# Performance work log

Measured on AMD Instinct MI355X. Metric: run time of the kernel, lower is better.

Reference implementation:

```python
import jax, jax.numpy as jnp
import numpy as np

N_CLASS = 100
HIDDEN = 768
BATCH = 512


def setup_inputs() -> dict:
    key = jax.random.key(0)
    kx, ky, km = jax.random.split(key, 3)
    x = jax.random.normal(kx, (BATCH, HIDDEN), dtype=jnp.float32)
    y = jax.random.randint(ky, (BATCH,), 0, N_CLASS, dtype=jnp.int64 if jax.config.jax_enable_x64 else jnp.int32)
    M = jax.random.normal(km, (N_CLASS, HIDDEN, HIDDEN), dtype=jnp.float32) * 0.1
    return {"x": x, "y": y, "M": M}


def _get_sym_M(M):
    # M: [n_class, H, H]
    h = M.shape[-1]
    Mt = jnp.triu(M)
    diag = Mt * jnp.eye(h, dtype=M.dtype)  # keeps only diagonal entries
    # detached ReLU correction: pushes near-zero/negative diagonal up by ~0.001
    Mt = Mt + jax.lax.stop_gradient(jax.nn.relu(-(diag - 0.001)))
    return jnp.einsum('chk,cjk->chj', Mt, Mt)  # Mt @ Mt^T, symmetric PSD


def reference(x, y, M):
    # Faithful to: one_hot(y) broadcast-select of sym_M then batched matvec.
    # Equivalent efficient form: gather selected class matrix, per-sample matvec.
    sym = _get_sym_M(M)            # [n_class, H, H]
    My = sym[y]                    # [B, H, H] gather (irregular access)
    return jnp.einsum('bh,bhk->bk', x, My)  # [B, H]
```

## Files before the change

### kernel.cpp

```cpp
#include <hip/hip_runtime.h>

#define NCLASS 100
#define HID    768
#define BATCH  512
#define SG     8
#define NPAN   12

__device__ __forceinline__ void build_list(const int* __restrict__ y, int c,
                                           int* slist, int* scnt, int t) {
    if (t < 64) {
        int n = 0;
        for (int r = 0; r < BATCH / 64; ++r) {
            const int b = r * 64 + t;
            const bool hit = (y[b] == c);
            const unsigned long long mask = __ballot(hit);
            if (hit) slist[n + __popcll(mask & ((1ull << t) - 1ull))] = b;
            n += __popcll(mask);
        }
        if (t == 0) *scnt = n;
    }
}

__global__ __launch_bounds__(256, 4) void kA(
    const float* __restrict__ x, const int* __restrict__ y,
    const float* __restrict__ M, float* __restrict__ T)
{
    const int c    = blockIdx.x;
    const int g    = (NPAN - 1) - blockIdx.y;
    const int t    = threadIdx.x;
    const int col0 = g * 64;

    __shared__ int   slist[BATCH];
    __shared__ int   scnt;
    __shared__ float xs[SG][HID];
    __shared__ float Xs[SG];
    __shared__ float red[4][16][4][SG];
    __shared__ float dj_lds[64];

    build_list(y, c, slist, &scnt, t);
    __syncthreads();
    const int cnt = scnt;
    if (cnt == 0) return;

    const float* __restrict__ Mc = M + (size_t)c * HID * HID;
    const int wv = t >> 6, ln = t & 63;
    const int hg = t >> 4, jq = t & 15;

    if (t < 64) {
        const int jg = col0 + t;
        dj_lds[t] = fmaxf(Mc[(size_t)jg * HID + jg], 1e-3f);
    }

    for (int g0 = 0; g0 < cnt; g0 += SG) {
        const int gs = min(SG, cnt - g0);
        __syncthreads();
        #pragma unroll
        for (int ss = 0; ss < 2; ++ss) {
            const int s = 2 * wv + ss;
            const int b = slist[g0 + (s < gs ? s : 0)];
            const float4* xr = (const float4*)(x + (size_t)b * HID);
            const float4 v0 = xr[ln], v1 = xr[ln + 64], v2 = xr[ln + 128];
            *(float4*)&xs[s][ln * 4]       = v0;
            *(float4*)&xs[s][ln * 4 + 256] = v1;
            *(float4*)&xs[s][ln * 4 + 512] = v2;
            float pX = ((v0.x + v0.y) + (v0.z + v0.w))
                     + ((v1.x + v1.y) + (v1.z + v1.w))
                     + ((v2.x + v2.y) + (v2.z + v2.w));
            #pragma unroll
            for (int off = 32; off; off >>= 1) pX += __shfl_xor(pX, off);
            if (ln == 0) Xs[s] = pX;
        }
        __syncthreads();

        float tp[4][SG];
        #pragma unroll
        for (int jj = 0; jj < 4; ++jj)
            #pragma unroll
            for (int s = 0; s < SG; ++s) tp[jj][s] = 0.f;

        for (int h = hg; h < col0 + 64; h += 16) {
            float4 mq = *(const float4*)(Mc + (size_t)h * HID + col0 + jq * 4);
            if (h >= col0) {
                const int hrel = h - col0;
                if (4 * jq + 0 <= hrel) mq.x = 0.f;
                if (4 * jq + 1 <= hrel) mq.y = 0.f;
                if (4 * jq + 2 <= hrel) mq.z = 0.f;
                if (4 * jq + 3 <= hrel) mq.w = 0.f;
            }
            #pragma unroll
            for (int s = 0; s < SG; ++s) {
                const float xv = xs[s][h];
                tp[0][s] = fmaf(xv, mq.x, tp[0][s]);
                tp[1][s] = fmaf(xv, mq.y, tp[1][s]);
                tp[2][s] = fmaf(xv, mq.z, tp[2][s]);
                tp[3][s] = fmaf(xv, mq.w, tp[3][s]);
            }
        }
        #pragma unroll
        for (int m = 16; m <= 32; m <<= 1)
            #pragma unroll
            for (int jj = 0; jj < 4; ++jj)
                #pragma unroll
                for (int s = 0; s < SG; ++s)
                    tp[jj][s] += __shfl_xor(tp[jj][s], m);
        if (ln < 16) {
            #pragma unroll
            for (int jj = 0; jj < 4; ++jj)
                #pragma unroll
                for (int s = 0; s < SG; ++s)
                    red[wv][ln][jj][s] = tp[jj][s];
        }
        __syncthreads();
        {
            const int j = t & 63, jq2 = j >> 2, jj2 = j & 3;
            const int jg = col0 + j;
            #pragma unroll
            for (int ss = 0; ss < 2; ++ss) {
                const int s = (t >> 6) * 2 + ss;
                if (s < gs) {
                    const float u = (red[0][jq2][jj2][s] + red[1][jq2][jj2][s])
                                  + (red[2][jq2][jj2][s] + red[3][jq2][jj2][s]);
                    const float xj = xs[s][jg];
                    T[(size_t)slist[g0 + s] * HID + jg] =
                        u + dj_lds[j] * xj + 1e-3f * (Xs[s] - xj);
                }
            }
        }
    }
}

__global__ __launch_bounds__(256, 4) void kB(
    const int* __restrict__ y, const float* __restrict__ M,
    const float* __restrict__ T, float* __restrict__ out)
{
    const int c  = blockIdx.x;
    const int q  = blockIdx.y;
    const int t  = threadIdx.x;
    const int k0 = q * 64;

    __shared__ int   slist[BATCH];
    __shared__ int   scnt;
    __shared__ float ts[SG][HID];
    __shared__ float Tt[SG];
    __shared__ float ob[SG][64];
    __shared__ float dk_lds[64];

    build_list(y, c, slist, &scnt, t);
    __syncthreads();
    const int cnt = scnt;
    if (cnt == 0) return;

    const float* __restrict__ Mc = M + (size_t)c * HID * HID;
    const int wv = t >> 6, ln = t & 63;
    const int kr = t >> 4, cg = t & 15;

    if (t < 64) {
        const int kg = k0 + t;
        dk_lds[t] = fmaxf(Mc[(size_t)kg * HID + kg], 1e-3f);
    }

    for (int g0 = 0; g0 < cnt; g0 += SG) {
        const int gs = min(SG, cnt - g0);
        __syncthreads();
        #pragma unroll
        for (int ss = 0; ss < 2; ++ss) {
            const int s = 2 * wv + ss;
            const int b = slist[g0 + (s < gs ? s : 0)];
            const float4* tr = (const float4*)(T + (size_t)b * HID);
            const float4 v0 = tr[ln], v1 = tr[ln + 64], v2 = tr[ln + 128];
            *(float4*)&ts[s][ln * 4]       = v0;
            *(float4*)&ts[s][ln * 4 + 256] = v1;
            *(float4*)&ts[s][ln * 4 + 512] = v2;
            float pT = ((v0.x + v0.y) + (v0.z + v0.w))
                     + ((v1.x + v1.y) + (v1.z + v1.w))
                     + ((v2.x + v2.y) + (v2.z + v2.w));
            #pragma unroll
            for (int off = 32; off; off >>= 1) pT += __shfl_xor(pT, off);
            if (ln == 0) Tt[s] = pT;
        }
        __syncthreads();

        float acc[4][SG];
        #pragma unroll
        for (int m = 0; m < 4; ++m)
            #pragma unroll
            for (int s = 0; s < SG; ++s) acc[m][s] = 0.f;

        for (int jb = k0; jb < HID; jb += 64) {
            const int j0 = jb + cg * 4;
            float4 mq[4];
            #pragma unroll
            for (int m = 0; m < 4; ++m) {
                const int k = k0 + 16 * m + kr;
                mq[m] = *(const float4*)(Mc + (size_t)k * HID + j0);
                if (jb == k0) {
                    if (j0 + 0 <= k) mq[m].x = 0.f;
                    if (j0 + 1 <= k) mq[m].y = 0.f;
                    if (j0 + 2 <= k) mq[m].z = 0.f;
                    if (j0 + 3 <= k) mq[m].w = 0.f;
                }
            }
            #pragma unroll
            for (int s = 0; s < SG; ++s) {
                const float4 tv = *(const float4*)&ts[s][j0];
                #pragma unroll
                for (int m = 0; m < 4; ++m) {
                    acc[m][s] = fmaf(mq[m].x, tv.x, acc[m][s]);
                    acc[m][s] = fmaf(mq[m].y, tv.y, acc[m][s]);
                    acc[m][s] = fmaf(mq[m].z, tv.z, acc[m][s]);
                    acc[m][s] = fmaf(mq[m].w, tv.w, acc[m][s]);
                }
            }
        }
        #pragma unroll
        for (int m2 = 1; m2 <= 8; m2 <<= 1)
            #pragma unroll
            for (int m = 0; m < 4; ++m)
                #pragma unroll
                for (int s = 0; s < SG; ++s)
                    acc[m][s] += __shfl_xor(acc[m][s], m2);
        if (cg == 0) {
            #pragma unroll
            for (int m = 0; m < 4; ++m)
                #pragma unroll
                for (int s = 0; s < SG; ++s)
                    ob[s][16 * m + kr] = acc[m][s];
        }
        __syncthreads();
        {
            const int j = t & 63;
            const int k = k0 + j;
            #pragma unroll
            for (int ss = 0; ss < 2; ++ss) {
                const int s = (t >> 6) * 2 + ss;
                if (s < gs) {
                    const float tk = ts[s][k];
                    out[(size_t)slist[g0 + s] * HID + k] =
                        ob[s][j] + dk_lds[j] * tk + 1e-3f * (Tt[s] - tk);
                }
            }
        }
    }
}

extern "C" void kernel_launch(void* const* d_in, const int* in_sizes, int n_in,
                              void* d_out, int out_size, void* d_ws, size_t ws_size,
                              hipStream_t stream) {
    const float* x = (const float*)d_in[0];
    const int*   y = (const int*)d_in[1];
    const float* M = (const float*)d_in[2];
    float* out = (float*)d_out;
    float* T   = (float*)d_ws;

    kA<<<dim3(NCLASS, NPAN), 256, 0, stream>>>(x, y, M, T);
    kB<<<dim3(NCLASS, NPAN), 256, 0, stream>>>(y, M, T, out);
}
```

Before: 87.05 us.

## Fuse both matvec stages per column panel with partial-sum buffer and final reduce kernel

```diff
diff --git a/kernel.cpp b/kernel.cpp
--- a/kernel.cpp
+++ b/kernel.cpp
@@ -4,7 +4,8 @@
 #define HID    768
 #define BATCH  512
 #define SG     8
-#define NPAN   12
+#define NPAIR  6
+#define BH     (BATCH * HID)
 
 __device__ __forceinline__ void build_list(const int* __restrict__ y, int c,
                                            int* slist, int* scnt, int t) {
@@ -21,21 +22,21 @@
     }
 }
 
-__global__ __launch_bounds__(256, 4) void kA(
+__global__ __launch_bounds__(256, 4) void fusedAB(
     const float* __restrict__ x, const int* __restrict__ y,
-    const float* __restrict__ M, float* __restrict__ T)
+    const float* __restrict__ M, float* __restrict__ T, float* __restrict__ P)
 {
-    const int c    = blockIdx.x;
-    const int g    = (NPAN - 1) - blockIdx.y;
-    const int t    = threadIdx.x;
-    const int col0 = g * 64;
+    const int c  = blockIdx.x;
+    const int pr = blockIdx.y;
+    const int t  = threadIdx.x;
 
     __shared__ int   slist[BATCH];
     __shared__ int   scnt;
     __shared__ float xs[SG][HID];
     __shared__ float Xs[SG];
-    __shared__ float red[4][16][4][SG];
-    __shared__ float dj_lds[64];
+    __shared__ float red[4][16][4][SG + 1];
+    __shared__ float t_lds[SG][64];
+    __shared__ float dj2[2][64];
 
     build_list(y, c, slist, &scnt, t);
     __syncthreads();
@@ -45,10 +46,13 @@
     const float* __restrict__ Mc = M + (size_t)c * HID * HID;
     const int wv = t >> 6, ln = t & 63;
     const int hg = t >> 4, jq = t & 15;
-
-    if (t < 64) {
-        const int jg = col0 + t;
-        dj_lds[t] = fmaxf(Mc[(size_t)jg * HID + jg], 1e-3f);
+    const int rr = t >> 2, qt = t & 3;
+
+    const int gtab[2] = {11 - pr, pr};
+    if (t < 128) {
+        const int pi = t >> 6;
+        const int jg = gtab[pi] * 64 + (t & 63);
+        dj2[pi][t & 63] = fmaxf(Mc[(size_t)jg * HID + jg], 1e-3f);
     }
 
     for (int g0 = 0; g0 < cnt; g0 += SG) {
@@ -72,174 +76,167 @@
         }
         __syncthreads();
 
-        float tp[4][SG];
-        #pragma unroll
-        for (int jj = 0; jj < 4; ++jj)
-            #pragma unroll
-            for (int s = 0; s < SG; ++s) tp[jj][s] = 0.f;
-
-        for (int h = hg; h < col0 + 64; h += 16) {
-            float4 mq = *(const float4*)(Mc + (size_t)h * HID + col0 + jq * 4);
-            if (h >= col0) {
-                const int hrel = h - col0;
-                if (4 * jq + 0 <= hrel) mq.x = 0.f;
-                if (4 * jq + 1 <= hrel) mq.y = 0.f;
-                if (4 * jq + 2 <= hrel) mq.z = 0.f;
-                if (4 * jq + 3 <= hrel) mq.w = 0.f;
-            }
-            #pragma unroll
-            for (int s = 0; s < SG; ++s) {
-                const float xv = xs[s][h];
-                tp[0][s] = fmaf(xv, mq.x, tp[0][s]);
-                tp[1][s] = fmaf(xv, mq.y, tp[1][s]);
-                tp[2][s] = fmaf(xv, mq.z, tp[2][s]);
-                tp[3][s] = fmaf(xv, mq.w, tp[3][s]);
-            }
-        }
-        #pragma unroll
-        for (int m = 16; m <= 32; m <<= 1)
+        for (int pi = 0; pi < 2; ++pi) {
+            const int g    = gtab[pi];
+            const int col0 = g * 64;
+            const float* __restrict__ Mpan = Mc + col0 + jq * 4;
+
+            float tp[4][SG];
             #pragma unroll
             for (int jj = 0; jj < 4; ++jj)
                 #pragma unroll
-                for (int s = 0; s < SG; ++s)
-                    tp[jj][s] += __shfl_xor(tp[jj][s], m);
-        if (ln < 16) {
+                for (int s = 0; s < SG; ++s) tp[jj][s] = 0.f;
+
+            for (int hb = 0; hb < col0; hb += 64) {
+                float4 ma[4];
+                #pragma unroll
+                for (int m = 0; m < 4; ++m)
+                    ma[m] = *(const float4*)(Mpan + (size_t)(hb + hg + 16 * m) * HID);
+                #pragma unroll
+                for (int m = 0; m < 4; ++m) {
+                    const int h = hb + hg + 16 * m;
+                    #pragma unroll
+                    for (int s = 0; s < SG; ++s) {
+                        const float xv = xs[s][h];
+                        tp[0][s] = fmaf(xv, ma[m].x, tp[0][s]);
+                        tp[1][s] = fmaf(xv, ma[m].y, tp[1][s]);
+                        tp[2][s] = fmaf(xv, ma[m].z, tp[2][s]);
+                        tp[3][s] = fmaf(xv, ma[m].w, tp[3][s]);
+                    }
+                }
+            }
+            {
+                float4 ma[4];
+                #pragma unroll
+                for (int m = 0; m < 4; ++m) {
+                    const int hrel = hg + 16 * m;
+                    ma[m] = *(const float4*)(Mpan + (size_t)(col0 + hrel) * HID);
+                    if (4 * jq + 0 <= hrel) ma[m].x = 0.f;
+                    if (4 * jq + 1 <= hrel) ma[m].y = 0.f;
+                    if (4 * jq + 2 <= hrel) ma[m].z = 0.f;
+                    if (4 * jq + 3 <= hrel) ma[m].w = 0.f;
+                }
+                #pragma unroll
+                for (int m = 0; m < 4; ++m) {
+                    const int h = col0 + hg + 16 * m;
+                    #pragma unroll
+                    for (int s = 0; s < SG; ++s) {
+                        const float xv = xs[s][h];
+                        tp[0][s] = fmaf(xv, ma[m].x, tp[0][s]);
+                        tp[1][s] = fmaf(xv, ma[m].y, tp[1][s]);
+                        tp[2][s] = fmaf(xv, ma[m].z, tp[2][s]);
+                        tp[3][s] = fmaf(xv, ma[m].w, tp[3][s]);
+                    }
+                }
+            }
             #pragma unroll
-            for (int jj = 0; jj < 4; ++jj)
-                #pragma unroll
-                for (int s = 0; s < SG; ++s)
-                    red[wv][ln][jj][s] = tp[jj][s];
-        }
-        __syncthreads();
-        {
-            const int j = t & 63, jq2 = j >> 2, jj2 = j & 3;
-            const int jg = col0 + j;
-            #pragma unroll
-            for (int ss = 0; ss < 2; ++ss) {
-                const int s = (t >> 6) * 2 + ss;
-                if (s < gs) {
+            for (int mm = 16; mm <= 32; mm <<= 1)
+                #pragma unroll
+                for (int jj = 0; jj < 4; ++jj)
+                    #pragma unroll
+                    for (int s = 0; s < SG; ++s)
+                        tp[jj][s] += __shfl_xor(tp[jj][s], mm);
+            if (ln < 16) {
+                #pragma unroll
+                for (int jj = 0; jj < 4; ++jj)
+                    #pragma unroll
+                    for (int s = 0; s < SG; ++s)
+                        red[wv][ln][jj][s] = tp[jj][s];
+            }
+            __syncthreads();
+            {
+                const int j = t & 63, jq2 = j >> 2, jj2 = j & 3;
+                const int jg = col0 + j;
+                #pragma unroll
+                for (int ss = 0; ss < 2; ++ss) {
+                    const int s = (t >> 6) * 2 + ss;
                     const float u = (red[0][jq2][jj2][s] + red[1][jq2][jj2][s])
                                   + (red[2][jq2][jj2][s] + red[3][jq2][jj2][s]);
                     const float xj = xs[s][jg];
-                    T[(size_t)slist[g0 + s] * HID + jg] =
-                        u + dj_lds[j] * xj + 1e-3f * (Xs[s] - xj);
-                }
-            }
+                    const float tj = u + dj2[pi][j] * xj + 1e-3f * (Xs[s] - xj);
+                    t_lds[s][j] = tj;
+                    if (s < gs)
+                        T[(size_t)slist[g0 + s] * HID + jg] = tj;
+                }
+            }
+            __syncthreads();
+
+            float* __restrict__ Pg = P + (size_t)g * BH;
+            for (int kb = 0; kb < col0 + 64; kb += 64) {
+                const int k = kb + rr;
+                const float* __restrict__ rowp = Mc + (size_t)k * HID + col0;
+                float4 mv[4];
+                #pragma unroll
+                for (int u = 0; u < 4; ++u)
+                    mv[u] = ((const float4*)rowp)[qt + 4 * u];
+                if (kb == col0) {
+                    #pragma unroll
+                    for (int u = 0; u < 4; ++u) {
+                        const int jb = 4 * (qt + 4 * u);
+                        if (jb + 0 <= rr) mv[u].x = 0.f;
+                        if (jb + 1 <= rr) mv[u].y = 0.f;
+                        if (jb + 2 <= rr) mv[u].z = 0.f;
+                        if (jb + 3 <= rr) mv[u].w = 0.f;
+                    }
+                }
+                float acc[SG];
+                #pragma unroll
+                for (int s = 0; s < SG; ++s) acc[s] = 0.f;
+                #pragma unroll
+                for (int s = 0; s < SG; ++s) {
+                    #pragma unroll
+                    for (int u = 0; u < 4; ++u) {
+                        const float4 tv = *(const float4*)&t_lds[s][4 * (qt + 4 * u)];
+                        acc[s] = fmaf(mv[u].x, tv.x, acc[s]);
+                        acc[s] = fmaf(mv[u].y, tv.y, acc[s]);
+                        acc[s] = fmaf(mv[u].z, tv.z, acc[s]);
+                        acc[s] = fmaf(mv[u].w, tv.w, acc[s]);
+                    }
+                }
+                #pragma unroll
+                for (int s = 0; s < SG; ++s) {
+                    acc[s] += __shfl_xor(acc[s], 1);
+                    acc[s] += __shfl_xor(acc[s], 2);
+                }
+                if (qt == 0) {
+                    for (int s = 0; s < gs; ++s)
+                        Pg[(size_t)slist[g0 + s] * HID + k] = acc[s];
+                }
+            }
+            __syncthreads();
         }
     }
 }
 
-__global__ __launch_bounds__(256, 4) void kB(
+__global__ __launch_bounds__(256, 4) void k3(
     const int* __restrict__ y, const float* __restrict__ M,
-    const float* __restrict__ T, float* __restrict__ out)
+    const float* __restrict__ T, const float* __restrict__ P,
+    float* __restrict__ out)
 {
-    const int c  = blockIdx.x;
-    const int q  = blockIdx.y;
-    const int t  = threadIdx.x;
-    const int k0 = q * 64;
-
-    __shared__ int   slist[BATCH];
-    __shared__ int   scnt;
-    __shared__ float ts[SG][HID];
-    __shared__ float Tt[SG];
-    __shared__ float ob[SG][64];
-    __shared__ float dk_lds[64];
-
-    build_list(y, c, slist, &scnt, t);
+    const int b = blockIdx.x;
+    const int t = threadIdx.x;
+    const int c = y[b];
+
+    __shared__ float wred[4];
+    const float* __restrict__ tb = T + (size_t)b * HID;
+    const float t0 = tb[t], t1 = tb[t + 256], t2 = tb[t + 512];
+    float s = t0 + t1 + t2;
+    #pragma unroll
+    for (int off = 32; off; off >>= 1) s += __shfl_xor(s, off);
+    if ((t & 63) == 0) wred[t >> 6] = s;
     __syncthreads();
-    const int cnt = scnt;
-    if (cnt == 0) return;
+    const float Tt = (wred[0] + wred[1]) + (wred[2] + wred[3]);
 
     const float* __restrict__ Mc = M + (size_t)c * HID * HID;
-    const int wv = t >> 6, ln = t & 63;
-    const int kr = t >> 4, cg = t & 15;
-
-    if (t < 64) {
-        const int kg = k0 + t;
-        dk_lds[t] = fmaxf(Mc[(size_t)kg * HID + kg], 1e-3f);
-    }
-
-    for (int g0 = 0; g0 < cnt; g0 += SG) {
-        const int gs = min(SG, cnt - g0);
-        __syncthreads();
-        #pragma unroll
-        for (int ss = 0; ss < 2; ++ss) {
-            const int s = 2 * wv + ss;
-            const int b = slist[g0 + (s < gs ? s : 0)];
-            const float4* tr = (const float4*)(T + (size_t)b * HID);
-            const float4 v0 = tr[ln], v1 = tr[ln + 64], v2 = tr[ln + 128];
-            *(float4*)&ts[s][ln * 4]       = v0;
-            *(float4*)&ts[s][ln * 4 + 256] = v1;
-            *(float4*)&ts[s][ln * 4 + 512] = v2;
-            float pT = ((v0.x + v0.y) + (v0.z + v0.w))
-                     + ((v1.x + v1.y) + (v1.z + v1.w))
-                     + ((v2.x + v2.y) + (v2.z + v2.w));
-            #pragma unroll
-            for (int off = 32; off; off >>= 1) pT += __shfl_xor(pT, off);
-            if (ln == 0) Tt[s] = pT;
-        }
-        __syncthreads();
-
-        float acc[4][SG];
-        #pragma unroll
-        for (int m = 0; m < 4; ++m)
-            #pragma unroll
-            for (int s = 0; s < SG; ++s) acc[m][s] = 0.f;
-
-        for (int jb = k0; jb < HID; jb += 64) {
-            const int j0 = jb + cg * 4;
-            float4 mq[4];
-            #pragma unroll
-            for (int m = 0; m < 4; ++m) {
-                const int k = k0 + 16 * m + kr;
-                mq[m] = *(const float4*)(Mc + (size_t)k * HID + j0);
-                if (jb == k0) {
-                    if (j0 + 0 <= k) mq[m].x = 0.f;
-                    if (j0 + 1 <= k) mq[m].y = 0.f;
-                    if (j0 + 2 <= k) mq[m].z = 0.f;
-                    if (j0 + 3 <= k) mq[m].w = 0.f;
-                }
-            }
-            #pragma unroll
-            for (int s = 0; s < SG; ++s) {
-                const float4 tv = *(const float4*)&ts[s][j0];
-                #pragma unroll
-                for (int m = 0; m < 4; ++m) {
-                    acc[m][s] = fmaf(mq[m].x, tv.x, acc[m][s]);
-                    acc[m][s] = fmaf(mq[m].y, tv.y, acc[m][s]);
-                    acc[m][s] = fmaf(mq[m].z, tv.z, acc[m][s]);
-                    acc[m][s] = fmaf(mq[m].w, tv.w, acc[m][s]);
-                }
-            }
-        }
-        #pragma unroll
-        for (int m2 = 1; m2 <= 8; m2 <<= 1)
-            #pragma unroll
-            for (int m = 0; m < 4; ++m)
-                #pragma unroll
-                for (int s = 0; s < SG; ++s)
-                    acc[m][s] += __shfl_xor(acc[m][s], m2);
-        if (cg == 0) {
-            #pragma unroll
-            for (int m = 0; m < 4; ++m)
-                #pragma unroll
-                for (int s = 0; s < SG; ++s)
-                    ob[s][16 * m + kr] = acc[m][s];
-        }
-        __syncthreads();
-        {
-            const int j = t & 63;
-            const int k = k0 + j;
-            #pragma unroll
-            for (int ss = 0; ss < 2; ++ss) {
-                const int s = (t >> 6) * 2 + ss;
-                if (s < gs) {
-                    const float tk = ts[s][k];
-                    out[(size_t)slist[g0 + s] * HID + k] =
-                        ob[s][j] + dk_lds[j] * tk + 1e-3f * (Tt[s] - tk);
-                }
-            }
-        }
+    const float tv[3] = {t0, t1, t2};
+    #pragma unroll
+    for (int q = 0; q < 3; ++q) {
+        const int k = t + 256 * q;
+        float pk = 0.f;
+        for (int p = k >> 6; p < 12; ++p)
+            pk += P[(size_t)p * BH + (size_t)b * HID + k];
+        const float dk = fmaxf(Mc[(size_t)k * HID + k], 1e-3f);
+        out[(size_t)b * HID + k] = pk + dk * tv[q] + 1e-3f * (Tt - tv[q]);
     }
 }
 
@@ -251,7 +248,8 @@
     const float* M = (const float*)d_in[2];
     float* out = (float*)d_out;
     float* T   = (float*)d_ws;
-
-    kA<<<dim3(NCLASS, NPAN), 256, 0, stream>>>(x, y, M, T);
-    kB<<<dim3(NCLASS, NPAN), 256, 0, stream>>>(y, M, T, out);
-}
+    float* P   = (float*)d_ws + BH;
+
+    fusedAB<<<dim3(NCLASS, NPAIR), 256, 0, stream>>>(x, y, M, T, P);
+    k3<<<dim3(BATCH), 256, 0, stream>>>(y, M, T, P, out);
+}
```

New measurement: 192.0 us. 2.21x slower.

## Split first triangular matvec by row bands with separate reduction kernel

Applied to the files above, without the earlier changes.

```diff
diff --git a/kernel.cpp b/kernel.cpp
--- a/kernel.cpp
+++ b/kernel.cpp
@@ -5,6 +5,9 @@
 #define BATCH  512
 #define SG     8
 #define NPAN   12
+#define BH     (BATCH * HID)
+
+__constant__ int hb_tab[13] = {0, 32, 68, 104, 140, 180, 224, 272, 324, 384, 456, 548, 768};
 
 __device__ __forceinline__ void build_list(const int* __restrict__ y, int c,
                                            int* slist, int* scnt, int t) {
@@ -21,21 +24,19 @@
     }
 }
 
-__global__ __launch_bounds__(256, 4) void kA(
+__global__ __launch_bounds__(192, 4) void kA2(
     const float* __restrict__ x, const int* __restrict__ y,
-    const float* __restrict__ M, float* __restrict__ T)
+    const float* __restrict__ M, float* __restrict__ Tp)
 {
-    const int c    = blockIdx.x;
-    const int g    = (NPAN - 1) - blockIdx.y;
+    const int c    = blockIdx.y;
+    const int rb   = blockIdx.x;
     const int t    = threadIdx.x;
-    const int col0 = g * 64;
+    const int h_lo = hb_tab[rb], h_hi = hb_tab[rb + 1];
+    const int W    = h_hi - h_lo;
 
     __shared__ int   slist[BATCH];
     __shared__ int   scnt;
-    __shared__ float xs[SG][HID];
-    __shared__ float Xs[SG];
-    __shared__ float red[4][16][4][SG];
-    __shared__ float dj_lds[64];
+    __shared__ float xs[SG][224];
 
     build_list(y, c, slist, &scnt, t);
     __syncthreads();
@@ -43,89 +44,90 @@
     if (cnt == 0) return;
 
     const float* __restrict__ Mc = M + (size_t)c * HID * HID;
-    const int wv = t >> 6, ln = t & 63;
-    const int hg = t >> 4, jq = t & 15;
-
-    if (t < 64) {
-        const int jg = col0 + t;
-        dj_lds[t] = fmaxf(Mc[(size_t)jg * HID + jg], 1e-3f);
-    }
+    const int jb = 4 * t;
 
     for (int g0 = 0; g0 < cnt; g0 += SG) {
         const int gs = min(SG, cnt - g0);
         __syncthreads();
-        #pragma unroll
-        for (int ss = 0; ss < 2; ++ss) {
-            const int s = 2 * wv + ss;
+        {
+            const int s = t / 24, l = t - s * 24;
             const int b = slist[g0 + (s < gs ? s : 0)];
-            const float4* xr = (const float4*)(x + (size_t)b * HID);
-            const float4 v0 = xr[ln], v1 = xr[ln + 64], v2 = xr[ln + 128];
-            *(float4*)&xs[s][ln * 4]       = v0;
-            *(float4*)&xs[s][ln * 4 + 256] = v1;
-            *(float4*)&xs[s][ln * 4 + 512] = v2;
-            float pX = ((v0.x + v0.y) + (v0.z + v0.w))
-                     + ((v1.x + v1.y) + (v1.z + v1.w))
-                     + ((v2.x + v2.y) + (v2.z + v2.w));
-            #pragma unroll
-            for (int off = 32; off; off >>= 1) pX += __shfl_xor(pX, off);
-            if (ln == 0) Xs[s] = pX;
-        }
-        __syncthreads();
-
-        float tp[4][SG];
-        #pragma unroll
-        for (int jj = 0; jj < 4; ++jj)
-            #pragma unroll
-            for (int s = 0; s < SG; ++s) tp[jj][s] = 0.f;
-
-        for (int h = hg; h < col0 + 64; h += 16) {
-            float4 mq = *(const float4*)(Mc + (size_t)h * HID + col0 + jq * 4);
-            if (h >= col0) {
-                const int hrel = h - col0;
-                if (4 * jq + 0 <= hrel) mq.x = 0.f;
-                if (4 * jq + 1 <= hrel) mq.y = 0.f;
-                if (4 * jq + 2 <= hrel) mq.z = 0.f;
-                if (4 * jq + 3 <= hrel) mq.w = 0.f;
-            }
+            const float4* xr = (const float4*)(x + (size_t)b * HID + h_lo);
+            #pragma unroll
+            for (int k2 = 0; k2 < 3; ++k2) {
+                const int idx = l + 24 * k2;
+                if (idx * 4 < W) *(float4*)&xs[s][idx * 4] = xr[idx];
+            }
+        }
+        __syncthreads();
+
+        float4 a[SG];
+        #pragma unroll
+        for (int s = 0; s < SG; ++s) { a[s].x = 0.f; a[s].y = 0.f; a[s].z = 0.f; a[s].w = 0.f; }
+
+        for (int h = h_lo; h < h_hi; h += 2) {
+            float4 m0, m1;
+            m0.x = m0.y = m0.z = m0.w = 0.f;
+            m1.x = m1.y = m1.z = m1.w = 0.f;
+            if (jb + 3 > h)     m0 = *(const float4*)(Mc + (size_t)h * HID + jb);
+            if (jb + 3 > h + 1) m1 = *(const float4*)(Mc + (size_t)(h + 1) * HID + jb);
+            if (jb + 0 <= h) m0.x = 0.f;
+            if (jb + 1 <= h) m0.y = 0.f;
+            if (jb + 2 <= h) m0.z = 0.f;
+            if (jb + 3 <= h) m0.w = 0.f;
+            if (jb + 0 <= h + 1) m1.x = 0.f;
+            if (jb + 1 <= h + 1) m1.y = 0.f;
+            if (jb + 2 <= h + 1) m1.z = 0.f;
+            if (jb + 3 <= h + 1) m1.w = 0.f;
+            const int hr = h - h_lo;
             #pragma unroll
             for (int s = 0; s < SG; ++s) {
-                const float xv = xs[s][h];
-                tp[0][s] = fmaf(xv, mq.x, tp[0][s]);
-                tp[1][s] = fmaf(xv, mq.y, tp[1][s]);
-                tp[2][s] = fmaf(xv, mq.z, tp[2][s]);
-                tp[3][s] = fmaf(xv, mq.w, tp[3][s]);
-            }
-        }
-        #pragma unroll
-        for (int m = 16; m <= 32; m <<= 1)
-            #pragma unroll
-            for (int jj = 0; jj < 4; ++jj)
-                #pragma unroll
-                for (int s = 0; s < SG; ++s)
-                    tp[jj][s] += __shfl_xor(tp[jj][s], m);
-        if (ln < 16) {
-            #pragma unroll
-            for (int jj = 0; jj < 4; ++jj)
-                #pragma unroll
-                for (int s = 0; s < SG; ++s)
-                    red[wv][ln][jj][s] = tp[jj][s];
-        }
-        __syncthreads();
-        {
-            const int j = t & 63, jq2 = j >> 2, jj2 = j & 3;
-            const int jg = col0 + j;
-            #pragma unroll
-            for (int ss = 0; ss < 2; ++ss) {
-                const int s = (t >> 6) * 2 + ss;
-                if (s < gs) {
-                    const float u = (red[0][jq2][jj2][s] + red[1][jq2][jj2][s])
-                                  + (red[2][jq2][jj2][s] + red[3][jq2][jj2][s]);
-                    const float xj = xs[s][jg];
-                    T[(size_t)slist[g0 + s] * HID + jg] =
-                        u + dj_lds[j] * xj + 1e-3f * (Xs[s] - xj);
-                }
-            }
-        }
+                const float x0 = xs[s][hr], x1 = xs[s][hr + 1];
+                a[s].x = fmaf(x0, m0.x, a[s].x);
+                a[s].y = fmaf(x0, m0.y, a[s].y);
+                a[s].z = fmaf(x0, m0.z, a[s].z);
+                a[s].w = fmaf(x0, m0.w, a[s].w);
+                a[s].x = fmaf(x1, m1.x, a[s].x);
+                a[s].y = fmaf(x1, m1.y, a[s].y);
+                a[s].z = fmaf(x1, m1.z, a[s].z);
+                a[s].w = fmaf(x1, m1.w, a[s].w);
+            }
+        }
+        float* __restrict__ Tpr = Tp + (size_t)rb * BH;
+        for (int s = 0; s < gs; ++s)
+            *(float4*)(Tpr + (size_t)slist[g0 + s] * HID + jb) = a[s];
+    }
+}
+
+__global__ __launch_bounds__(256) void kT(
+    const float* __restrict__ x, const int* __restrict__ y,
+    const float* __restrict__ M, const float* __restrict__ Tp,
+    float* __restrict__ T)
+{
+    const int b = blockIdx.x, t = threadIdx.x;
+    const int c = y[b];
+    __shared__ float wred[4];
+
+    const size_t bh = (size_t)b * HID;
+    const float xv0 = x[bh + t], xv1 = x[bh + t + 256], xv2 = x[bh + t + 512];
+    float sx = xv0 + xv1 + xv2;
+    #pragma unroll
+    for (int off = 32; off; off >>= 1) sx += __shfl_xor(sx, off);
+    if ((t & 63) == 0) wred[t >> 6] = sx;
+    __syncthreads();
+    const float X = (wred[0] + wred[1]) + (wred[2] + wred[3]);
+
+    const float* __restrict__ Mc = M + (size_t)c * HID * HID;
+    const float xx[3] = {xv0, xv1, xv2};
+    #pragma unroll
+    for (int qi = 0; qi < 3; ++qi) {
+        const int j = t + 256 * qi;
+        float u = 0.f;
+        #pragma unroll
+        for (int rb = 0; rb < 12; ++rb)
+            u += Tp[(size_t)rb * BH + bh + j];
+        const float dj = fmaxf(Mc[(size_t)j * (HID + 1)], 1e-3f);
+        T[bh + j] = u + dj * xx[qi] + 1e-3f * (X - xx[qi]);
     }
 }
 
@@ -133,8 +135,8 @@
     const int* __restrict__ y, const float* __restrict__ M,
     const float* __restrict__ T, float* __restrict__ out)
 {
-    const int c  = blockIdx.x;
-    const int q  = blockIdx.y;
+    const int c  = blockIdx.y;
+    const int q  = blockIdx.x;
     const int t  = threadIdx.x;
     const int k0 = q * 64;
 
@@ -186,14 +188,14 @@
             #pragma unroll
             for (int s = 0; s < SG; ++s) acc[m][s] = 0.f;
 
-        for (int jb = k0; jb < HID; jb += 64) {
-            const int j0 = jb + cg * 4;
+        for (int jbq = k0; jbq < HID; jbq += 64) {
+            const int j0 = jbq + cg * 4;
             float4 mq[4];
             #pragma unroll
             for (int m = 0; m < 4; ++m) {
                 const int k = k0 + 16 * m + kr;
                 mq[m] = *(const float4*)(Mc + (size_t)k * HID + j0);
-                if (jb == k0) {
+                if (jbq == k0) {
                     if (j0 + 0 <= k) mq[m].x = 0.f;
                     if (j0 + 1 <= k) mq[m].y = 0.f;
                     if (j0 + 2 <= k) mq[m].z = 0.f;
@@ -250,8 +252,11 @@
     const int*   y = (const int*)d_in[1];
     const float* M = (const float*)d_in[2];
     float* out = (float*)d_out;
-    float* T   = (float*)d_ws;
-
-    kA<<<dim3(NCLASS, NPAN), 256, 0, stream>>>(x, y, M, T);
-    kB<<<dim3(NCLASS, NPAN), 256, 0, stream>>>(y, M, T, out);
-}
+
+    float* Tp = (float*)d_ws;
+    float* T  = (float*)d_ws + 12 * (size_t)BH;
+
+    kA2<<<dim3(12, NCLASS), 192, 0, stream>>>(x, y, M, Tp);
+    kT<<<dim3(BATCH), 256, 0, stream>>>(x, y, M, Tp, T);
+    kB<<<dim3(NPAN, NCLASS), 256, 0, stream>>>(y, M, T, out);
+}
```

Result: slower. 163.5 us (+87.8%).

## Double-buffer M panel loads in registers and swap grid dimension order

Applied to the files above, without the earlier changes.

```diff
diff --git a/kernel.cpp b/kernel.cpp
--- a/kernel.cpp
+++ b/kernel.cpp
@@ -25,10 +25,11 @@
     const float* __restrict__ x, const int* __restrict__ y,
     const float* __restrict__ M, float* __restrict__ T)
 {
-    const int c    = blockIdx.x;
-    const int g    = (NPAN - 1) - blockIdx.y;
+    const int c    = blockIdx.y;
+    const int g    = (NPAN - 1) - blockIdx.x;
     const int t    = threadIdx.x;
     const int col0 = g * 64;
+    const int nch  = g + 1;
 
     __shared__ int   slist[BATCH];
     __shared__ int   scnt;
@@ -42,7 +43,8 @@
     const int cnt = scnt;
     if (cnt == 0) return;
 
-    const float* __restrict__ Mc = M + (size_t)c * HID * HID;
+    const float* __restrict__ Mc   = M + (size_t)c * HID * HID;
+    const float* __restrict__ Mpan = Mc + col0 + (t & 15) * 4;
     const int wv = t >> 6, ln = t & 63;
     const int hg = t >> 4, jq = t & 15;
 
@@ -50,6 +52,37 @@
         const int jg = col0 + t;
         dj_lds[t] = fmaxf(Mc[(size_t)jg * HID + jg], 1e-3f);
     }
+
+#define KA_LOAD(R0, R1, R2, R3, ci)                                          \
+    {   const size_t rb_ = (size_t)((ci) * 64 + hg);                         \
+        R0 = *(const float4*)(Mpan + (rb_     ) * HID);                      \
+        R1 = *(const float4*)(Mpan + (rb_ + 16) * HID);                      \
+        R2 = *(const float4*)(Mpan + (rb_ + 32) * HID);                      \
+        R3 = *(const float4*)(Mpan + (rb_ + 48) * HID); }
+
+#define KA_MASK1(R, mi)                                                      \
+    {   const int hrel_ = hg + 16 * (mi);                                    \
+        if (4 * jq + 0 <= hrel_) R.x = 0.f;                                  \
+        if (4 * jq + 1 <= hrel_) R.y = 0.f;                                  \
+        if (4 * jq + 2 <= hrel_) R.z = 0.f;                                  \
+        if (4 * jq + 3 <= hrel_) R.w = 0.f; }
+
+#define KA_FMA1(R, mi, ci)                                                   \
+    {   const int h_ = (ci) * 64 + hg + 16 * (mi);                           \
+        _Pragma("unroll")                                                    \
+        for (int s = 0; s < SG; ++s) {                                       \
+            const float xv_ = xs[s][h_];                                     \
+            tp[0][s] = fmaf(xv_, R.x, tp[0][s]);                             \
+            tp[1][s] = fmaf(xv_, R.y, tp[1][s]);                             \
+            tp[2][s] = fmaf(xv_, R.z, tp[2][s]);                             \
+            tp[3][s] = fmaf(xv_, R.w, tp[3][s]);                             \
+        } }
+
+#define KA_COMP(R0, R1, R2, R3, ci)                                          \
+    { KA_FMA1(R0, 0, ci) KA_FMA1(R1, 1, ci) KA_FMA1(R2, 2, ci) KA_FMA1(R3, 3, ci) }
+
+#define KA_MASKD(R0, R1, R2, R3)                                             \
+    { KA_MASK1(R0, 0) KA_MASK1(R1, 1) KA_MASK1(R2, 2) KA_MASK1(R3, 3) }
 
     for (int g0 = 0; g0 < cnt; g0 += SG) {
         const int gs = min(SG, cnt - g0);
@@ -78,24 +111,21 @@
             #pragma unroll
             for (int s = 0; s < SG; ++s) tp[jj][s] = 0.f;
 
-        for (int h = hg; h < col0 + 64; h += 16) {
-            float4 mq = *(const float4*)(Mc + (size_t)h * HID + col0 + jq * 4);
-            if (h >= col0) {
-                const int hrel = h - col0;
-                if (4 * jq + 0 <= hrel) mq.x = 0.f;
-                if (4 * jq + 1 <= hrel) mq.y = 0.f;
-                if (4 * jq + 2 <= hrel) mq.z = 0.f;
-                if (4 * jq + 3 <= hrel) mq.w = 0.f;
-            }
-            #pragma unroll
-            for (int s = 0; s < SG; ++s) {
-                const float xv = xs[s][h];
-                tp[0][s] = fmaf(xv, mq.x, tp[0][s]);
-                tp[1][s] = fmaf(xv, mq.y, tp[1][s]);
-                tp[2][s] = fmaf(xv, mq.z, tp[2][s]);
-                tp[3][s] = fmaf(xv, mq.w, tp[3][s]);
-            }
-        }
+        float4 A0, A1, A2, A3, B0, B1, B2, B3;
+        KA_LOAD(A0, A1, A2, A3, 0)
+        int ci = 0;
+        for (; ci + 2 <= nch; ci += 2) {
+            KA_LOAD(B0, B1, B2, B3, ci + 1)
+            KA_COMP(A0, A1, A2, A3, ci)
+            if (ci + 2 < nch) KA_LOAD(A0, A1, A2, A3, ci + 2)
+            if (ci + 1 == nch - 1) KA_MASKD(B0, B1, B2, B3)
+            KA_COMP(B0, B1, B2, B3, ci + 1)
+        }
+        if (ci < nch) {
+            KA_MASKD(A0, A1, A2, A3)
+            KA_COMP(A0, A1, A2, A3, ci)
+        }
+
         #pragma unroll
         for (int m = 16; m <= 32; m <<= 1)
             #pragma unroll
@@ -127,16 +157,22 @@
             }
         }
     }
+#undef KA_LOAD
+#undef KA_MASK1
+#undef KA_FMA1
+#undef KA_COMP
+#undef KA_MASKD
 }
 
 __global__ __launch_bounds__(256, 4) void kB(
     const int* __restrict__ y, const float* __restrict__ M,
     const float* __restrict__ T, float* __restrict__ out)
 {
-    const int c  = blockIdx.x;
-    const int q  = blockIdx.y;
-    const int t  = threadIdx.x;
-    const int k0 = q * 64;
+    const int c   = blockIdx.y;
+    const int q   = blockIdx.x;
+    const int t   = threadIdx.x;
+    const int k0  = q * 64;
+    const int nch = NPAN - q;
 
     __shared__ int   slist[BATCH];
     __shared__ int   scnt;
@@ -158,6 +194,46 @@
         const int kg = k0 + t;
         dk_lds[t] = fmaxf(Mc[(size_t)kg * HID + kg], 1e-3f);
     }
+
+#define KB_LOAD(R0, R1, R2, R3, ci)                                          \
+    {   const size_t jo_ = (size_t)(k0 + (ci) * 64 + cg * 4);                \
+        R0 = *(const float4*)(Mc + (size_t)(k0 + kr     ) * HID + jo_);      \
+        R1 = *(const float4*)(Mc + (size_t)(k0 + kr + 16) * HID + jo_);      \
+        R2 = *(const float4*)(Mc + (size_t)(k0 + kr + 32) * HID + jo_);      \
+        R3 = *(const float4*)(Mc + (size_t)(k0 + kr + 48) * HID + jo_); }
+
+#define KB_MASK1(R, mi)                                                      \
+    {   const int k_ = k0 + 16 * (mi) + kr, j0_ = k0 + cg * 4;               \
+        if (j0_ + 0 <= k_) R.x = 0.f;                                        \
+        if (j0_ + 1 <= k_) R.y = 0.f;                                        \
+        if (j0_ + 2 <= k_) R.z = 0.f;                                        \
+        if (j0_ + 3 <= k_) R.w = 0.f; }
+
+#define KB_COMP(R0, R1, R2, R3, ci)                                          \
+    {   const int j0_ = k0 + (ci) * 64 + cg * 4;                             \
+        _Pragma("unroll")                                                    \
+        for (int s = 0; s < SG; ++s) {                                       \
+            const float4 tv_ = *(const float4*)&ts[s][j0_];                  \
+            acc[0][s] = fmaf(R0.x, tv_.x, acc[0][s]);                        \
+            acc[0][s] = fmaf(R0.y, tv_.y, acc[0][s]);                        \
+            acc[0][s] = fmaf(R0.z, tv_.z, acc[0][s]);                        \
+            acc[0][s] = fmaf(R0.w, tv_.w, acc[0][s]);                        \
+            acc[1][s] = fmaf(R1.x, tv_.x, acc[1][s]);                        \
+            acc[1][s] = fmaf(R1.y, tv_.y, acc[1][s]);                        \
+            acc[1][s] = fmaf(R1.z, tv_.z, acc[1][s]);                        \
+            acc[1][s] = fmaf(R1.w, tv_.w, acc[1][s]);                        \
+            acc[2][s] = fmaf(R2.x, tv_.x, acc[2][s]);                        \
+            acc[2][s] = fmaf(R2.y, tv_.y, acc[2][s]);                        \
+            acc[2][s] = fmaf(R2.z, tv_.z, acc[2][s]);                        \
+            acc[2][s] = fmaf(R2.w, tv_.w, acc[2][s]);                        \
+            acc[3][s] = fmaf(R3.x, tv_.x, acc[3][s]);                        \
+            acc[3][s] = fmaf(R3.y, tv_.y, acc[3][s]);                        \
+            acc[3][s] = fmaf(R3.z, tv_.z, acc[3][s]);                        \
+            acc[3][s] = fmaf(R3.w, tv_.w, acc[3][s]);                        \
+        } }
+
+#define KB_MASKD(R0, R1, R2, R3)                                             \
+    { KB_MASK1(R0, 0) KB_MASK1(R1, 1) KB_MASK1(R2, 2) KB_MASK1(R3, 3) }
 
     for (int g0 = 0; g0 < cnt; g0 += SG) {
         const int gs = min(SG, cnt - g0);
@@ -186,32 +262,21 @@
             #pragma unroll
             for (int s = 0; s < SG; ++s) acc[m][s] = 0.f;
 
-        for (int jb = k0; jb < HID; jb += 64) {
-            const int j0 = jb + cg * 4;
-            float4 mq[4];
-            #pragma unroll
-            for (int m = 0; m < 4; ++m) {
-                const int k = k0 + 16 * m + kr;
-                mq[m] = *(const float4*)(Mc + (size_t)k * HID + j0);
-                if (jb == k0) {
-                    if (j0 + 0 <= k) mq[m].x = 0.f;
-                    if (j0 + 1 <= k) mq[m].y = 0.f;
-                    if (j0 + 2 <= k) mq[m].z = 0.f;
-                    if (j0 + 3 <= k) mq[m].w = 0.f;
-                }
-            }
-            #pragma unroll
-            for (int s = 0; s < SG; ++s) {
-                const float4 tv = *(const float4*)&ts[s][j0];
-                #pragma unroll
-                for (int m = 0; m < 4; ++m) {
-                    acc[m][s] = fmaf(mq[m].x, tv.x, acc[m][s]);
-                    acc[m][s] = fmaf(mq[m].y, tv.y, acc[m][s]);
-                    acc[m][s] = fmaf(mq[m].z, tv.z, acc[m][s]);
-                    acc[m][s] = fmaf(mq[m].w, tv.w, acc[m][s]);
-                }
-            }
-        }
+        float4 A0, A1, A2, A3, B0, B1, B2, B3;
+        KB_LOAD(A0, A1, A2, A3, 0)
+        int ci = 0;
+        for (; ci + 2 <= nch; ci += 2) {
+            KB_LOAD(B0, B1, B2, B3, ci + 1)
+            if (ci == 0) KB_MASKD(A0, A1, A2, A3)
+            KB_COMP(A0, A1, A2, A3, ci)
+            if (ci + 2 < nch) KB_LOAD(A0, A1, A2, A3, ci + 2)
+            KB_COMP(B0, B1, B2, B3, ci + 1)
+        }
+        if (ci < nch) {
+            if (ci == 0) KB_MASKD(A0, A1, A2, A3)
+            KB_COMP(A0, A1, A2, A3, ci)
+        }
+
         #pragma unroll
         for (int m2 = 1; m2 <= 8; m2 <<= 1)
             #pragma unroll
@@ -241,6 +306,10 @@
             }
         }
     }
+#undef KB_LOAD
+#undef KB_MASK1
+#undef KB_COMP
+#undef KB_MASKD
 }
 
 extern "C" void kernel_launch(void* const* d_in, const int* in_sizes, int n_in,
@@ -252,6 +321,6 @@
     float* out = (float*)d_out;
     float* T   = (float*)d_ws;
 
-    kA<<<dim3(NCLASS, NPAN), 256, 0, stream>>>(x, y, M, T);
-    kB<<<dim3(NCLASS, NPAN), 256, 0, stream>>>(y, M, T, out);
+    kA<<<dim3(NPAN, NCLASS), 256, 0, stream>>>(x, y, M, T);
+    kB<<<dim3(NPAN, NCLASS), 256, 0, stream>>>(y, M, T, out);
 }
```

Result: slower. 141.5 us (+62.6%).
